# Performance work log

Hardware: AMD Instinct MI355X
Metric: run time of the kernel (lower is better)

Reference implementation:

```python
import jax, jax.numpy as jnp
import numpy as np

V, D = 50000, 300          # word vocab / embedding dim
P, M = 8, 512              # number of POS experts / candidates per expert
B, L, HS = 8, 1024, 512    # batch, seq len, ctx feature size (ctx_fs*2)
N_POS_TOTAL = 16           # POS alphabet size; experts cover ids 0..P-1
EPS = 1e-12


def setup_inputs() -> dict:
    key = jax.random.key(0)
    ks = jax.random.split(key, 8)
    inp_word = jax.random.randint(ks[0], (B, L), 0, V)
    inp_pos = jax.random.randint(ks[1], (B, L), 0, N_POS_TOTAL)
    ctx = jax.random.normal(ks[2], (B, L, HS), dtype=jnp.float32)
    word_emb_weight = jax.random.normal(ks[3], (V, D), dtype=jnp.float32)
    dec_W = jax.random.normal(ks[4], (P, HS, M), dtype=jnp.float32) * (1.0 / np.sqrt(HS))
    dec_b = jax.random.normal(ks[5], (P, M), dtype=jnp.float32) * 0.01
    tgt_words = jax.random.randint(ks[6], (P, M), 0, V)
    u = jax.random.uniform(ks[7], (P, B * L, M), dtype=jnp.float32, minval=1e-8, maxval=1.0 - 1e-8)
    gumbel = -jnp.log(-jnp.log(u))  # standard Gumbel(0,1) noise
    return {"inp_word": inp_word, "inp_pos": inp_pos, "ctx": ctx,
            "word_emb_weight": word_emb_weight, "dec_W": dec_W, "dec_b": dec_b,
            "tgt_words": tgt_words, "gumbel": gumbel}


def reference(inp_word, inp_pos, ctx, word_emb_weight, dec_W, dec_b, tgt_words, gumbel):
    t = 1.0  # eval-mode temperature (get_temperature only in training)
    T = B * L
    ctx2 = ctx.reshape(T, HS)
    word_flat = inp_word.reshape(T)
    pos_flat = inp_pos.reshape(T)

    # per-POS expert decode: Linear + Softmax, then log(p + eps)   [P, T, M]
    logits = jnp.einsum('td,pdm->ptm', ctx2, dec_W) + dec_b[:, None, :]
    pspt = jnp.log(jax.nn.softmax(logits, axis=-1) + EPS)
    # gumbel-softmax sample
    sft = jax.nn.softmax((pspt + gumbel) / t, axis=-1)            # [P, T, M]
    y = jnp.argmax(sft, axis=-1)                                  # [P, T]
    y_word = jnp.take_along_axis(tgt_words, y, axis=1)            # map wid -> word id, [P, T]
    tgt_emb = word_emb_weight[tgt_words]                          # [P, M, D]
    x_emb = jnp.einsum('ptm,pmd->ptd', sft, tgt_emb)              # [P, T, D]

    # masked scatter back by POS routing
    sel = (pos_flat[None, :] == jnp.arange(P, dtype=pos_flat.dtype)[:, None])  # [P, T]
    msk = pos_flat < P                                            # union of expert masks
    nn_msk = pos_flat < 2                                         # POS ids 0,1 play the 'NN*' role

    word_new = jnp.sum(jnp.where(sel, y_word, 0), axis=0)
    emb_new = jnp.einsum('pt,ptd->td', sel.astype(x_emb.dtype), x_emb)

    obf_word = jnp.where(msk, word_new, word_flat).reshape(B, L)
    base_emb = word_emb_weight[word_flat]
    obf_word_emb = jnp.where(msk[:, None], emb_new, base_emb).reshape(B, L, D)
    obf_mask = msk.astype(jnp.float32).reshape(B, L)
    nn_mask = nn_msk.reshape(B, L)
    return obf_word, obf_word_emb, obf_mask, nn_mask
```

## Files before the change

kernel.cpp:

```cpp
#include <hip/hip_runtime.h>
#include <cstddef>

#define T_TOT 8192
#define M_    512
#define HS_   512
#define D_    300
#define P_    8
#define TT    4
#define CNT_STRIDE 16

__global__ __launch_bounds__(256) void route_kernel(
    const int* __restrict__ inp_word, const int* __restrict__ inp_pos,
    int* __restrict__ cnt, int* __restrict__ perm,
    float* __restrict__ out_word, float* __restrict__ out_maskm,
    float* __restrict__ out_maskn)
{
    __shared__ int lcnt[P_];
    __shared__ int lbase[P_];
    int tid = threadIdx.x;
    int t = blockIdx.x * 256 + tid;
    if (tid < P_) lcnt[tid] = 0;
    __syncthreads();

    int pp = inp_pos[t];
    out_maskm[t] = (pp < P_) ? 1.0f : 0.0f;
    out_maskn[t] = (pp < 2)  ? 1.0f : 0.0f;
    int loc = 0;
    if (pp < P_) {
        loc = atomicAdd(&lcnt[pp], 1);
    } else {
        out_word[t] = (float)inp_word[t];
    }
    __syncthreads();
    if (tid < P_) lbase[tid] = atomicAdd(&cnt[tid * CNT_STRIDE], lcnt[tid]);
    __syncthreads();
    if (pp < P_) perm[pp * T_TOT + lbase[pp] + loc] = t;
}

__global__ __launch_bounds__(128) void base_emb_kernel(
    const int* __restrict__ inp_word, const int* __restrict__ inp_pos,
    const float* __restrict__ wemb, float* __restrict__ out_emb)
{
    int t = blockIdx.x;
    if (inp_pos[t] < P_) return;
    int w = inp_word[t];
    if (threadIdx.x < 75) {
        float4 v = *(const float4*)&wemb[(size_t)w * D_ + threadIdx.x * 4];
        *(float4*)&out_emb[(size_t)t * D_ + threadIdx.x * 4] = v;
    }
}

__global__ __launch_bounds__(256, 4) void expert_kernel(
    const float* __restrict__ ctx,   const float* __restrict__ wemb,
    const float* __restrict__ dec_W, const float* __restrict__ dec_b,
    const int*   __restrict__ tgt,   const float* __restrict__ gumbel,
    const int*   __restrict__ cnt,   const int*   __restrict__ perm,
    float* __restrict__ out_word,    float* __restrict__ out_emb)
{
    int p = blockIdx.x;
    int count = cnt[p * CNT_STRIDE];
    int start = blockIdx.y * TT;
    if (start >= count) return;
    int n = min(TT, count - start);

    __shared__ float buf[TT][M_];
    __shared__ int   tok_ids[TT];
    __shared__ int   tw_s[M_];

    int tn = threadIdx.x;
    if (tn < TT) tok_ids[tn] = (tn < n) ? perm[p * T_TOT + start + tn] : -1;
    tw_s[tn]       = tgt[p * M_ + tn];
    tw_s[tn + 256] = tgt[p * M_ + tn + 256];
    __syncthreads();

    #pragma unroll
    for (int it = 0; it < 2; ++it) {
        int idx  = tn + it * 256;
        int tok  = idx >> 7;
        int pos4 = idx & 127;
        int t = tok_ids[tok];
        float4 v = make_float4(0.f, 0.f, 0.f, 0.f);
        if (t >= 0) v = *(const float4*)&ctx[(size_t)t * HS_ + pos4 * 4];
        *(float4*)&buf[tok][pos4 * 4] = v;
    }
    __syncthreads();

    const float* Wp = dec_W + (size_t)p * HS_ * M_;
    int m0 = tn * 2;
    float accA[TT], accB[TT];
    #pragma unroll
    for (int k = 0; k < TT; ++k) { accA[k] = 0.f; accB[k] = 0.f; }

    for (int h4 = 0; h4 < HS_ / 4; ++h4) {
        float2 w0 = *(const float2*)&Wp[(size_t)(h4 * 4 + 0) * M_ + m0];
        float2 w1 = *(const float2*)&Wp[(size_t)(h4 * 4 + 1) * M_ + m0];
        float2 w2 = *(const float2*)&Wp[(size_t)(h4 * 4 + 2) * M_ + m0];
        float2 w3 = *(const float2*)&Wp[(size_t)(h4 * 4 + 3) * M_ + m0];
        #pragma unroll
        for (int k = 0; k < TT; ++k) {
            float4 c = *(const float4*)&buf[k][h4 * 4];
            accA[k] = fmaf(c.x, w0.x, fmaf(c.y, w1.x, fmaf(c.z, w2.x, fmaf(c.w, w3.x, accA[k]))));
            accB[k] = fmaf(c.x, w0.y, fmaf(c.y, w1.y, fmaf(c.z, w2.y, fmaf(c.w, w3.y, accB[k]))));
        }
    }
    __syncthreads();

    float b0 = dec_b[p * M_ + m0];
    float b1 = dec_b[p * M_ + m0 + 1];
    #pragma unroll
    for (int k = 0; k < TT; ++k) {
        *(float2*)&buf[k][m0] = make_float2(accA[k] + b0, accB[k] + b1);
    }
    __syncthreads();

    int wave = tn >> 6, lane = tn & 63;
    int tok = wave;
    if (tok < n) {
        int t = tok_ids[tok];
        float l[8];
        #pragma unroll
        for (int j = 0; j < 8; ++j) l[j] = buf[tok][j * 64 + lane];
        float mx = l[0];
        #pragma unroll
        for (int j = 1; j < 8; ++j) mx = fmaxf(mx, l[j]);
        for (int off = 32; off; off >>= 1) mx = fmaxf(mx, __shfl_xor(mx, off, 64));

        float ex[8];
        float se = 0.f;
        #pragma unroll
        for (int j = 0; j < 8; ++j) { ex[j] = expf(l[j] - mx); se += ex[j]; }
        for (int off = 32; off; off >>= 1) se += __shfl_xor(se, off, 64);

        const float* gp = gumbel + ((size_t)p * T_TOT + t) * M_;
        float s[8];
        float bm = -3.0e38f;
        int   bi = 0x7fffffff;
        #pragma unroll
        for (int j = 0; j < 8; ++j) {
            float q  = ex[j] / se;
            float sv = logf(q + 1e-12f) + gp[j * 64 + lane];
            s[j] = sv;
            if (sv > bm) { bm = sv; bi = j * 64 + lane; }
        }
        for (int off = 32; off; off >>= 1) {
            float ov = __shfl_xor(bm, off, 64);
            int   oi = __shfl_xor(bi, off, 64);
            if (ov > bm || (ov == bm && oi < bi)) { bm = ov; bi = oi; }
        }

        float e2[8];
        float s2 = 0.f;
        #pragma unroll
        for (int j = 0; j < 8; ++j) { e2[j] = expf(s[j] - bm); s2 += e2[j]; }
        for (int off = 32; off; off >>= 1) s2 += __shfl_xor(s2, off, 64);

        #pragma unroll
        for (int j = 0; j < 8; ++j) buf[tok][j * 64 + lane] = e2[j] / s2;

        if (lane == 0) out_word[t] = (float)tw_s[bi];
    }
    __syncthreads();

    if (tn < 150) {
        int d0 = tn * 2;
        float acA[TT], acB[TT];
        #pragma unroll
        for (int k = 0; k < TT; ++k) { acA[k] = 0.f; acB[k] = 0.f; }

        #pragma unroll 2
        for (int m4 = 0; m4 < M_ / 4; ++m4) {
            int t0 = tw_s[m4 * 4 + 0];
            int t1 = tw_s[m4 * 4 + 1];
            int t2 = tw_s[m4 * 4 + 2];
            int t3 = tw_s[m4 * 4 + 3];
            float2 e0  = *(const float2*)&wemb[(size_t)t0 * D_ + d0];
            float2 e1  = *(const float2*)&wemb[(size_t)t1 * D_ + d0];
            float2 e2v = *(const float2*)&wemb[(size_t)t2 * D_ + d0];
            float2 e3  = *(const float2*)&wemb[(size_t)t3 * D_ + d0];
            #pragma unroll
            for (int k = 0; k < TT; ++k) {
                float4 sv = *(const float4*)&buf[k][m4 * 4];
                acA[k] = fmaf(sv.x, e0.x, fmaf(sv.y, e1.x, fmaf(sv.z, e2v.x, fmaf(sv.w, e3.x, acA[k]))));
                acB[k] = fmaf(sv.x, e0.y, fmaf(sv.y, e1.y, fmaf(sv.z, e2v.y, fmaf(sv.w, e3.y, acB[k]))));
            }
        }
        #pragma unroll
        for (int k = 0; k < TT; ++k) {
            if (k < n) {
                int t = tok_ids[k];
                *(float2*)&out_emb[(size_t)t * D_ + d0] = make_float2(acA[k], acB[k]);
            }
        }
    }
}

extern "C" void kernel_launch(void* const* d_in, const int* in_sizes, int n_in,
                              void* d_out, int out_size, void* d_ws, size_t ws_size,
                              hipStream_t stream)
{
    const int*   inp_word = (const int*)d_in[0];
    const int*   inp_pos  = (const int*)d_in[1];
    const float* ctx      = (const float*)d_in[2];
    const float* wemb     = (const float*)d_in[3];
    const float* dec_W    = (const float*)d_in[4];
    const float* dec_b    = (const float*)d_in[5];
    const int*   tgt      = (const int*)d_in[6];
    const float* gumbel   = (const float*)d_in[7];

    float* out       = (float*)d_out;
    float* out_word  = out;
    float* out_emb   = out + T_TOT;
    float* out_maskm = out + T_TOT + T_TOT * D_;
    float* out_maskn = out_maskm + T_TOT;

    int* cnt  = (int*)d_ws;
    int* perm = cnt + P_ * CNT_STRIDE;

    hipMemsetAsync(d_ws, 0, P_ * CNT_STRIDE * sizeof(int), stream);
    route_kernel<<<T_TOT / 256, 256, 0, stream>>>(
        inp_word, inp_pos, cnt, perm, out_word, out_maskm, out_maskn);
    base_emb_kernel<<<T_TOT, 128, 0, stream>>>(inp_word, inp_pos, wemb, out_emb);
    expert_kernel<<<dim3(P_, T_TOT / TT), 256, 0, stream>>>(
        ctx, wemb, dec_W, dec_b, tgt, gumbel, cnt, perm, out_word, out_emb);
}
```

Measured before the change: 363.9 us.

## Double-buffer expert weights in LDS via async global_load_lds and double token tile

Doubles the tokens per block from 4 to 8, which halves how often each expert's weight matrix is re-read from global memory. Weight rows are now staged into a double-buffered LDS tile with asynchronous global-to-LDS loads, so the next slice can load while the current one is used. Each wave now handles two tokens' softmax/gumbel work, and the occupancy hint drops from 4 to 3 blocks per SU because of the larger LDS footprint. The grid launch still uses T_TOT/TT, so there are fewer blocks. The code relies on __syncthreads to cover completion of the async LDS loads, with no explicit vmcnt wait, which is a correctness risk.

```diff
diff --git a/kernel.cpp b/kernel.cpp
--- a/kernel.cpp
+++ b/kernel.cpp
@@ -6,8 +6,16 @@
 #define HS_   512
 #define D_    300
 #define P_    8
-#define TT    4
+#define TT    8
+#define KSTEP 8
+#define NSTEP (HS_ / KSTEP)
 #define CNT_STRIDE 16
+
+__device__ __forceinline__ void gload_lds16(const float* g, float* l) {
+    __builtin_amdgcn_global_load_lds(
+        (const __attribute__((address_space(1))) unsigned int*)g,
+        (__attribute__((address_space(3))) unsigned int*)l, 16, 0, 0);
+}
 
 __global__ __launch_bounds__(256) void route_kernel(
     const int* __restrict__ inp_word, const int* __restrict__ inp_pos,
@@ -50,7 +58,7 @@
     }
 }
 
-__global__ __launch_bounds__(256, 4) void expert_kernel(
+__global__ __launch_bounds__(256, 3) void expert_kernel(
     const float* __restrict__ ctx,   const float* __restrict__ wemb,
     const float* __restrict__ dec_W, const float* __restrict__ dec_b,
     const int*   __restrict__ tgt,   const float* __restrict__ gumbel,
@@ -63,7 +71,8 @@
     if (start >= count) return;
     int n = min(TT, count - start);
 
-    __shared__ float buf[TT][M_];
+    __shared__ float ctxb[TT][HS_];
+    __shared__ float wbuf[2][KSTEP][M_];
     __shared__ int   tok_ids[TT];
     __shared__ int   tw_s[M_];
 
@@ -73,53 +82,70 @@
     tw_s[tn + 256] = tgt[p * M_ + tn + 256];
     __syncthreads();
 
-    #pragma unroll
-    for (int it = 0; it < 2; ++it) {
+    const float* Wp = dec_W + (size_t)p * HS_ * M_;
+
+    #pragma unroll
+    for (int r = 0; r < 4; ++r)
+        gload_lds16(Wp + r * 1024 + tn * 4, &wbuf[0][0][0] + r * 1024 + tn * 4);
+
+    #pragma unroll
+    for (int it = 0; it < 4; ++it) {
         int idx  = tn + it * 256;
         int tok  = idx >> 7;
         int pos4 = idx & 127;
         int t = tok_ids[tok];
         float4 v = make_float4(0.f, 0.f, 0.f, 0.f);
         if (t >= 0) v = *(const float4*)&ctx[(size_t)t * HS_ + pos4 * 4];
-        *(float4*)&buf[tok][pos4 * 4] = v;
-    }
-    __syncthreads();
-
-    const float* Wp = dec_W + (size_t)p * HS_ * M_;
+        *(float4*)&ctxb[tok][pos4 * 4] = v;
+    }
+    __syncthreads();
+
     int m0 = tn * 2;
     float accA[TT], accB[TT];
     #pragma unroll
     for (int k = 0; k < TT; ++k) { accA[k] = 0.f; accB[k] = 0.f; }
 
-    for (int h4 = 0; h4 < HS_ / 4; ++h4) {
-        float2 w0 = *(const float2*)&Wp[(size_t)(h4 * 4 + 0) * M_ + m0];
-        float2 w1 = *(const float2*)&Wp[(size_t)(h4 * 4 + 1) * M_ + m0];
-        float2 w2 = *(const float2*)&Wp[(size_t)(h4 * 4 + 2) * M_ + m0];
-        float2 w3 = *(const float2*)&Wp[(size_t)(h4 * 4 + 3) * M_ + m0];
-        #pragma unroll
-        for (int k = 0; k < TT; ++k) {
-            float4 c = *(const float4*)&buf[k][h4 * 4];
-            accA[k] = fmaf(c.x, w0.x, fmaf(c.y, w1.x, fmaf(c.z, w2.x, fmaf(c.w, w3.x, accA[k]))));
-            accB[k] = fmaf(c.x, w0.y, fmaf(c.y, w1.y, fmaf(c.z, w2.y, fmaf(c.w, w3.y, accB[k]))));
-        }
-    }
-    __syncthreads();
+    int cur = 0;
+    for (int step = 0; step < NSTEP; ++step) {
+        if (step + 1 < NSTEP) {
+            const float* src = Wp + (size_t)(step + 1) * KSTEP * M_;
+            float* dst = &wbuf[cur ^ 1][0][0];
+            #pragma unroll
+            for (int r = 0; r < 4; ++r)
+                gload_lds16(src + r * 1024 + tn * 4, dst + r * 1024 + tn * 4);
+        }
+        #pragma unroll
+        for (int h4 = 0; h4 < KSTEP / 4; ++h4) {
+            float2 w0 = *(const float2*)&wbuf[cur][h4 * 4 + 0][m0];
+            float2 w1 = *(const float2*)&wbuf[cur][h4 * 4 + 1][m0];
+            float2 w2 = *(const float2*)&wbuf[cur][h4 * 4 + 2][m0];
+            float2 w3 = *(const float2*)&wbuf[cur][h4 * 4 + 3][m0];
+            #pragma unroll
+            for (int k = 0; k < TT; ++k) {
+                float4 c = *(const float4*)&ctxb[k][step * KSTEP + h4 * 4];
+                accA[k] = fmaf(c.x, w0.x, fmaf(c.y, w1.x, fmaf(c.z, w2.x, fmaf(c.w, w3.x, accA[k]))));
+                accB[k] = fmaf(c.x, w0.y, fmaf(c.y, w1.y, fmaf(c.z, w2.y, fmaf(c.w, w3.y, accB[k]))));
+            }
+        }
+        __syncthreads();
+        cur ^= 1;
+    }
 
     float b0 = dec_b[p * M_ + m0];
     float b1 = dec_b[p * M_ + m0 + 1];
     #pragma unroll
     for (int k = 0; k < TT; ++k) {
-        *(float2*)&buf[k][m0] = make_float2(accA[k] + b0, accB[k] + b1);
+        *(float2*)&ctxb[k][m0] = make_float2(accA[k] + b0, accB[k] + b1);
     }
     __syncthreads();
 
     int wave = tn >> 6, lane = tn & 63;
-    int tok = wave;
-    if (tok < n) {
+    for (int tok = wave * 2; tok < wave * 2 + 2; ++tok) {
+        if (tok >= n) continue;
         int t = tok_ids[tok];
         float l[8];
         #pragma unroll
-        for (int j = 0; j < 8; ++j) l[j] = buf[tok][j * 64 + lane];
+        for (int j = 0; j < 8; ++j) l[j] = ctxb[tok][j * 64 + lane];
         float mx = l[0];
         #pragma unroll
         for (int j = 1; j < 8; ++j) mx = fmaxf(mx, l[j]);
@@ -155,7 +181,7 @@
         for (int off = 32; off; off >>= 1) s2 += __shfl_xor(s2, off, 64);
 
         #pragma unroll
-        for (int j = 0; j < 8; ++j) buf[tok][j * 64 + lane] = e2[j] / s2;
+        for (int j = 0; j < 8; ++j) ctxb[tok][j * 64 + lane] = e2[j] / s2;
 
         if (lane == 0) out_word[t] = (float)tw_s[bi];
     }
@@ -179,7 +205,7 @@
             float2 e3  = *(const float2*)&wemb[(size_t)t3 * D_ + d0];
             #pragma unroll
             for (int k = 0; k < TT; ++k) {
-                float4 sv = *(const float4*)&buf[k][m4 * 4];
+                float4 sv = *(const float4*)&ctxb[k][m4 * 4];
                 acA[k] = fmaf(sv.x, e0.x, fmaf(sv.y, e1.x, fmaf(sv.z, e2v.x, fmaf(sv.w, e3.x, acA[k]))));
                 acB[k] = fmaf(sv.x, e0.y, fmaf(sv.y, e1.y, fmaf(sv.z, e2v.y, fmaf(sv.w, e3.y, acB[k]))));
             }
```

Result: faster. 340.3 us (-6.5%).

## Process 8 tokens per block with 512 threads, one output column per thread

Applied to the files above, without the earlier changes.

Doubles the number of tokens per expert block from 4 to 8 and the block size to 512 threads, so each thread now computes one logit column and one embedding dimension instead of two. Each dec_W and gathered embedding row is then reused across twice as many tokens, which halves the redundant weight and embedding traffic per token. The trade-offs are more registers and shared memory per block, a larger block, and scalar rather than float2 loads. With few tokens per expert the last block of each expert is more likely to be partly empty.

```diff
diff --git a/kernel.cpp b/kernel.cpp
--- a/kernel.cpp
+++ b/kernel.cpp
@@ -6,7 +6,7 @@
 #define HS_   512
 #define D_    300
 #define P_    8
-#define TT    4
+#define TT    8
 #define CNT_STRIDE 16
 
 __global__ __launch_bounds__(256) void route_kernel(
@@ -50,7 +50,7 @@
     }
 }
 
-__global__ __launch_bounds__(256, 4) void expert_kernel(
+__global__ __launch_bounds__(512, 4) void expert_kernel(
     const float* __restrict__ ctx,   const float* __restrict__ wemb,
     const float* __restrict__ dec_W, const float* __restrict__ dec_b,
     const int*   __restrict__ tgt,   const float* __restrict__ gumbel,
@@ -63,54 +63,49 @@
     if (start >= count) return;
     int n = min(TT, count - start);
 
-    __shared__ float buf[TT][M_];
+    __shared__ float ctxb[TT][HS_];
     __shared__ int   tok_ids[TT];
     __shared__ int   tw_s[M_];
 
     int tn = threadIdx.x;
     if (tn < TT) tok_ids[tn] = (tn < n) ? perm[p * T_TOT + start + tn] : -1;
-    tw_s[tn]       = tgt[p * M_ + tn];
-    tw_s[tn + 256] = tgt[p * M_ + tn + 256];
+    tw_s[tn & 511] = tgt[p * M_ + (tn & 511)];
     __syncthreads();
 
     #pragma unroll
     for (int it = 0; it < 2; ++it) {
-        int idx  = tn + it * 256;
+        int idx  = tn + it * 512;
         int tok  = idx >> 7;
         int pos4 = idx & 127;
         int t = tok_ids[tok];
         float4 v = make_float4(0.f, 0.f, 0.f, 0.f);
         if (t >= 0) v = *(const float4*)&ctx[(size_t)t * HS_ + pos4 * 4];
-        *(float4*)&buf[tok][pos4 * 4] = v;
-    }
-    __syncthreads();
-
-    const float* Wp = dec_W + (size_t)p * HS_ * M_;
-    int m0 = tn * 2;
-    float accA[TT], accB[TT];
+        *(float4*)&ctxb[tok][pos4 * 4] = v;
+    }
+    __syncthreads();
+
+    const float* Wp = dec_W + (size_t)p * HS_ * M_ + tn;
+    float acc[TT];
     #pragma unroll
-    for (int k = 0; k < TT; ++k) { accA[k] = 0.f; accB[k] = 0.f; }
-
+    for (int k = 0; k < TT; ++k) acc[k] = 0.f;
+
+    #pragma unroll 2
     for (int h4 = 0; h4 < HS_ / 4; ++h4) {
-        float2 w0 = *(const float2*)&Wp[(size_t)(h4 * 4 + 0) * M_ + m0];
-        float2 w1 = *(const float2*)&Wp[(size_t)(h4 * 4 + 1) * M_ + m0];
-        float2 w2 = *(const float2*)&Wp[(size_t)(h4 * 4 + 2) * M_ + m0];
-        float2 w3 = *(const float2*)&Wp[(size_t)(h4 * 4 + 3) * M_ + m0];
+        float w0 = Wp[(size_t)(h4 * 4 + 0) * M_];
+        float w1 = Wp[(size_t)(h4 * 4 + 1) * M_];
+        float w2 = Wp[(size_t)(h4 * 4 + 2) * M_];
+        float w3 = Wp[(size_t)(h4 * 4 + 3) * M_];
         #pragma unroll
         for (int k = 0; k < TT; ++k) {
-            float4 c = *(const float4*)&buf[k][h4 * 4];
-            accA[k] = fmaf(c.x, w0.x, fmaf(c.y, w1.x, fmaf(c.z, w2.x, fmaf(c.w, w3.x, accA[k]))));
-            accB[k] = fmaf(c.x, w0.y, fmaf(c.y, w1.y, fmaf(c.z, w2.y, fmaf(c.w, w3.y, accB[k]))));
-        }
-    }
-    __syncthreads();
-
-    float b0 = dec_b[p * M_ + m0];
-    float b1 = dec_b[p * M_ + m0 + 1];
+            float4 c = *(const float4*)&ctxb[k][h4 * 4];
+            acc[k] = fmaf(c.x, w0, fmaf(c.y, w1, fmaf(c.z, w2, fmaf(c.w, w3, acc[k]))));
+        }
+    }
+    __syncthreads();
+
+    float bb = dec_b[p * M_ + tn];
     #pragma unroll
-    for (int k = 0; k < TT; ++k) {
-        *(float2*)&buf[k][m0] = make_float2(accA[k] + b0, accB[k] + b1);
-    }
+    for (int k = 0; k < TT; ++k) ctxb[k][tn] = acc[k] + bb;
     __syncthreads();
 
     int wave = tn >> 6, lane = tn & 63;
@@ -119,7 +114,7 @@
         int t = tok_ids[tok];
         float l[8];
         #pragma unroll
-        for (int j = 0; j < 8; ++j) l[j] = buf[tok][j * 64 + lane];
+        for (int j = 0; j < 8; ++j) l[j] = ctxb[tok][j * 64 + lane];
         float mx = l[0];
         #pragma unroll
         for (int j = 1; j < 8; ++j) mx = fmaxf(mx, l[j]);
@@ -155,40 +150,39 @@
         for (int off = 32; off; off >>= 1) s2 += __shfl_xor(s2, off, 64);
 
         #pragma unroll
-        for (int j = 0; j < 8; ++j) buf[tok][j * 64 + lane] = e2[j] / s2;
+        for (int j = 0; j < 8; ++j) ctxb[tok][j * 64 + lane] = e2[j] / s2;
 
         if (lane == 0) out_word[t] = (float)tw_s[bi];
     }
     __syncthreads();
 
-    if (tn < 150) {
-        int d0 = tn * 2;
-        float acA[TT], acB[TT];
-        #pragma unroll
-        for (int k = 0; k < TT; ++k) { acA[k] = 0.f; acB[k] = 0.f; }
-
-        #pragma unroll 2
+    if (tn < D_) {
+        int d0 = tn;
+        float ac[TT];
+        #pragma unroll
+        for (int k = 0; k < TT; ++k) ac[k] = 0.f;
+
+        #pragma unroll 4
         for (int m4 = 0; m4 < M_ / 4; ++m4) {
             int t0 = tw_s[m4 * 4 + 0];
             int t1 = tw_s[m4 * 4 + 1];
             int t2 = tw_s[m4 * 4 + 2];
             int t3 = tw_s[m4 * 4 + 3];
-            float2 e0  = *(const float2*)&wemb[(size_t)t0 * D_ + d0];
-            float2 e1  = *(const float2*)&wemb[(size_t)t1 * D_ + d0];
-            float2 e2v = *(const float2*)&wemb[(size_t)t2 * D_ + d0];
-            float2 e3  = *(const float2*)&wemb[(size_t)t3 * D_ + d0];
+            float e0 = wemb[(size_t)t0 * D_ + d0];
+            float e1 = wemb[(size_t)t1 * D_ + d0];
+            float e2 = wemb[(size_t)t2 * D_ + d0];
+            float e3 = wemb[(size_t)t3 * D_ + d0];
             #pragma unroll
             for (int k = 0; k < TT; ++k) {
-                float4 sv = *(const float4*)&buf[k][m4 * 4];
-                acA[k] = fmaf(sv.x, e0.x, fmaf(sv.y, e1.x, fmaf(sv.z, e2v.x, fmaf(sv.w, e3.x, acA[k]))));
-                acB[k] = fmaf(sv.x, e0.y, fmaf(sv.y, e1.y, fmaf(sv.z, e2v.y, fmaf(sv.w, e3.y, acB[k]))));
+                float4 sv = *(const float4*)&ctxb[k][m4 * 4];
+                ac[k] = fmaf(sv.x, e0, fmaf(sv.y, e1, fmaf(sv.z, e2, fmaf(sv.w, e3, ac[k]))));
             }
         }
         #pragma unroll
         for (int k = 0; k < TT; ++k) {
             if (k < n) {
                 int t = tok_ids[k];
-                *(float2*)&out_emb[(size_t)t * D_ + d0] = make_float2(acA[k], acB[k]);
+                out_emb[(size_t)t * D_ + d0] = ac[k];
             }
         }
     }
@@ -220,6 +214,6 @@
     route_kernel<<<T_TOT / 256, 256, 0, stream>>>(
         inp_word, inp_pos, cnt, perm, out_word, out_maskm, out_maskn);
     base_emb_kernel<<<T_TOT, 128, 0, stream>>>(inp_word, inp_pos, wemb, out_emb);
-    expert_kernel<<<dim3(P_, T_TOT / TT), 256, 0, stream>>>(
+    expert_kernel<<<dim3(P_, T_TOT / TT), 512, 0, stream>>>(
         ctx, wemb, dec_W, dec_b, tgt, gumbel, cnt, perm, out_word, out_emb);
 }
```

Result: slower. 425.1 us (+16.8%).
